# Performance work log

Hardware: AMD Instinct MI355X
Metric: run time of the kernel (lower is better)

The kernel has to match this reference:

```python
import jax, jax.numpy as jnp
import numpy as np

B, T, C = 2, 2048, 2048
N_HEAD = 16
N_KV_HEAD = 16
HEAD_DIM = C // N_HEAD  # 128
KV_LORA = C // 2        # 1024
KV_PE = KV_LORA // 4    # 256
KV_CONTENT = KV_LORA - KV_PE  # 768
EPS = 1.1920929e-07  # torch.finfo(float32).eps, F.rms_norm default


def _rms_norm(x):
    # unlearned RMSNorm over last dim
    return x * jax.lax.rsqrt(jnp.mean(x * x, axis=-1, keepdims=True) + EPS)


def _apply_rotary(x, cos, sin):
    # x: (B,T,H,D); cos,sin: (1,T,1,D/2)
    d = x.shape[-1] // 2
    x1, x2 = x[..., :d], x[..., d:]
    return jnp.concatenate([x1 * cos + x2 * sin, -x1 * sin + x2 * cos], axis=-1)


def setup_inputs() -> dict:
    key = jax.random.key(0)
    ks = jax.random.split(key, 9)
    x = jax.random.normal(ks[0], (B, T, C), dtype=jnp.float32)
    # realistic RoPE tables (values bounded like real cos/sin)
    half = HEAD_DIM // 2
    inv_freq = 1.0 / (10000.0 ** (np.arange(0, half, dtype=np.float32) / half))
    tpos = np.arange(T, dtype=np.float32)
    ang = np.einsum('t,d->td', tpos, inv_freq)
    cos = jnp.asarray(np.cos(ang))[None, :, None, :]
    sin = jnp.asarray(np.sin(ang))[None, :, None, :]
    s = 0.02
    wq_a = jax.random.normal(ks[1], (C, KV_LORA), dtype=jnp.float32) * s
    wq_b = jax.random.normal(ks[2], (KV_LORA, N_HEAD * HEAD_DIM), dtype=jnp.float32) * s
    wkv_a = jax.random.normal(ks[3], (C, KV_LORA), dtype=jnp.float32) * s
    wk_b = jax.random.normal(ks[4], (KV_CONTENT, N_KV_HEAD * HEAD_DIM), dtype=jnp.float32) * s
    wkpe_b = jax.random.normal(ks[5], (KV_PE, N_KV_HEAD * HEAD_DIM), dtype=jnp.float32) * s
    wv_b = jax.random.normal(ks[6], (KV_CONTENT, N_KV_HEAD * HEAD_DIM), dtype=jnp.float32) * s
    wo = jax.random.normal(ks[7], (C, C), dtype=jnp.float32) * s
    return dict(x=x, cos=cos, sin=sin, wq_a=wq_a, wq_b=wq_b, wkv_a=wkv_a,
                wk_b=wk_b, wkpe_b=wkpe_b, wv_b=wv_b, wo=wo)


def reference(x, cos, sin, wq_a, wq_b, wkv_a, wk_b, wkpe_b, wv_b, wo):
    Bx, Tx, Cx = x.shape
    # low-rank Q path
    q = (x @ wq_a) @ wq_b                      # (B,T,H*D)
    q = q.reshape(Bx, Tx, N_HEAD, HEAD_DIM)
    # low-rank KV path with pe/content split
    kv_latent = x @ wkv_a                       # (B,T,KV_LORA)
    kv_pe = kv_latent[..., :KV_PE]
    kv_content = kv_latent[..., KV_PE:]
    k_content = (kv_content @ wk_b).reshape(Bx, Tx, N_KV_HEAD, HEAD_DIM)
    k_pe = (kv_pe @ wkpe_b).reshape(Bx, Tx, N_KV_HEAD, HEAD_DIM)
    k = k_content + _apply_rotary(k_pe, cos, sin)
    v = (kv_content @ wv_b).reshape(Bx, Tx, N_KV_HEAD, HEAD_DIM)
    # QK RMSNorm (unlearned)
    q = _rms_norm(q)
    k = _rms_norm(k)
    # SDPA, causal (kv_cache=None path); n_head == n_kv_head
    qh = q.transpose(0, 2, 1, 3)  # (B,H,T,D)
    kh = k.transpose(0, 2, 1, 3)
    vh = v.transpose(0, 2, 1, 3)
    scale = 1.0 / jnp.sqrt(jnp.asarray(HEAD_DIM, dtype=x.dtype))
    scores = jnp.einsum('bhqd,bhkd->bhqk', qh, kh) * scale
    causal = jnp.tril(jnp.ones((Tx, Tx), dtype=bool))
    scores = jnp.where(causal[None, None], scores, jnp.asarray(-jnp.inf, dtype=scores.dtype))
    probs = jax.nn.softmax(scores, axis=-1)
    y = jnp.einsum('bhqk,bhkd->bhqd', probs, vh)
    y = y.transpose(0, 2, 1, 3).reshape(Bx, Tx, Cx)
    return y @ wo
```

## Files before the change

### kernel.cpp

```cpp
#include <hip/hip_runtime.h>
#include <cstddef>
#include <cstdint>

#define TT 2048
#define HH 16
#define EPSV 1.1920929e-07f
#define QSCALE 0.08838834764831845f
#define LOG2E 1.4426950408889634f
#define THRL 11.0f

typedef short bfv8 __attribute__((ext_vector_type(8)));
typedef short bfv4 __attribute__((ext_vector_type(4)));
typedef float f32x4 __attribute__((ext_vector_type(4)));
typedef unsigned u32x2 __attribute__((ext_vector_type(2)));

__device__ __forceinline__ short f2bf(float f) {
    unsigned u = __builtin_bit_cast(unsigned, f);
    u += 0x7FFFu + ((u >> 16) & 1u);
    return (short)(u >> 16);
}
__device__ __forceinline__ float bf2f(short s) {
    unsigned u = ((unsigned)(unsigned short)s) << 16;
    return __builtin_bit_cast(float, u);
}
__device__ __forceinline__ bfv8 pack8(const float4 a, const float4 b) {
    bfv8 r;
    r[0]=f2bf(a.x); r[1]=f2bf(a.y); r[2]=f2bf(a.z); r[3]=f2bf(a.w);
    r[4]=f2bf(b.x); r[5]=f2bf(b.y); r[6]=f2bf(b.z); r[7]=f2bf(b.w);
    return r;
}
__device__ __forceinline__ void gload16(const void* g, void* l) {
    __builtin_amdgcn_global_load_lds(
        (const __attribute__((address_space(1))) unsigned int*)g,
        (__attribute__((address_space(3))) unsigned int*)l, 16, 0, 0);
}
__device__ __forceinline__ unsigned cvtpk(float a, float b) {
    unsigned r;
    asm("v_cvt_pk_bf16_f32 %0, %1, %2" : "=v"(r) : "v"(a), "v"(b));
    return r;
}
__device__ __forceinline__ float fexp2(float x) {
    float y;
    asm volatile("v_exp_f32 %0, %1\n\ts_nop 1" : "=v"(y) : "v"(x));
    return y;
}
__device__ __forceinline__ float bperm(float v, int addr) {
    return __builtin_bit_cast(float,
        __builtin_amdgcn_ds_bpermute(addr, __builtin_bit_cast(int, v)));
}
__device__ __forceinline__ bfv4 mkfrag(float a, float b, float c, float d) {
    u32x2 t; t[0] = cvtpk(a, b); t[1] = cvtpk(c, d);
    return __builtin_bit_cast(bfv4, t);
}

struct TransDesc { const float* src; short* dst; int R, C, b0; };
struct TransArgs { TransDesc t[7]; };

__global__ __launch_bounds__(256) void pre_all(TransArgs ta,
    const float* __restrict__ xsrc, short* __restrict__ xdst, int nx)
{
    __shared__ short tile[64][72];
    int bid = blockIdx.x;
    if (bid < nx) {
        const int i = bid * 256 + threadIdx.x;
        float4 a = ((const float4*)xsrc)[2 * i], b = ((const float4*)xsrc)[2 * i + 1];
        ((bfv8*)xdst)[i] = pack8(a, b);
        return;
    }
    bid -= nx;
    int e = 0;
#pragma unroll
    for (int k = 1; k < 7; ++k) if (bid >= ta.t[k].b0) e = k;
    const TransDesc D = ta.t[e];
    const int loc = bid - D.b0;
    const int cb = D.C >> 6;
    const int by = loc / cb, bx = loc - by * cb;
    const int tid = threadIdx.x;
    const int r0 = by * 64, c0 = bx * 64;
    {
        const int i = tid >> 2, c = (tid & 3) * 16;
        const float* sp = D.src + ((size_t)(r0 + i)) * D.C + c0 + c;
        float4 v0 = ((const float4*)sp)[0], v1 = ((const float4*)sp)[1];
        float4 v2 = ((const float4*)sp)[2], v3 = ((const float4*)sp)[3];
        *(bfv8*)&tile[i][c]     = pack8(v0, v1);
        *(bfv8*)&tile[i][c + 8] = pack8(v2, v3);
    }
    __syncthreads();
    {
        const int j = tid >> 2, rc = (tid & 3) * 16;
        bfv8 g0, g1;
#pragma unroll
        for (int jj = 0; jj < 8; ++jj) { g0[jj] = tile[rc + jj][j]; g1[jj] = tile[rc + 8 + jj][j]; }
        short* dp = D.dst + ((size_t)(c0 + j)) * D.R + r0 + rc;
        *(bfv8*)dp       = g0;
        *(bfv8*)(dp + 8) = g1;
    }
}

template<int OUT_MODE>
__global__ __launch_bounds__(256) void gemm_bf16(
    const short* __restrict__ A, int lda,
    const short* __restrict__ B, int ldb,
    void* __restrict__ Cptr, int ldc, int K)
{
    __shared__ short As[2][128 * 32];
    __shared__ short Bs[2][128 * 32];
    const int tid = threadIdx.x;
    const int w = tid >> 6, lane = tid & 63;
    const int lr = lane & 15, lg = lane >> 4;
    const int wr = w >> 1, wc = w & 1;
    const size_t bm = (size_t)blockIdx.y * 128, bn = (size_t)blockIdx.x * 128;

    f32x4 acc[4][4] = {};

    const int r0 = tid >> 2, ch = (tid & 3) * 8;
    const short* aB0 = A + (bm + r0) * (size_t)lda + ch;
    const short* aB1 = aB0 + 64 * (size_t)lda;
    const short* bB0 = B + (bn + r0) * (size_t)ldb + ch;
    const short* bB1 = bB0 + 64 * (size_t)ldb;
    const int wof = w * 512;

    gload16(aB0, As[0] + wof);
    gload16(aB1, As[0] + wof + 2048);
    gload16(bB0, Bs[0] + wof);
    gload16(bB1, Bs[0] + wof + 2048);
    __syncthreads();

    int cur = 0;
    for (int k0 = 0; k0 < K; k0 += 32) {
        if (k0 + 32 < K) {
            gload16(aB0 + k0 + 32, As[cur ^ 1] + wof);
            gload16(aB1 + k0 + 32, As[cur ^ 1] + wof + 2048);
            gload16(bB0 + k0 + 32, Bs[cur ^ 1] + wof);
            gload16(bB1 + k0 + 32, Bs[cur ^ 1] + wof + 2048);
        }
        bfv8 af[4], bfr[4];
#pragma unroll
        for (int i = 0; i < 4; ++i) {
            af[i]  = *(const bfv8*)&As[cur][(wr * 64 + i * 16 + lr) * 32 + lg * 8];
            bfr[i] = *(const bfv8*)&Bs[cur][(wc * 64 + i * 16 + lr) * 32 + lg * 8];
        }
#pragma unroll
        for (int i = 0; i < 4; ++i)
#pragma unroll
            for (int j = 0; j < 4; ++j)
                acc[i][j] = __builtin_amdgcn_mfma_f32_16x16x32_bf16(af[i], bfr[j], acc[i][j], 0, 0, 0);
        __syncthreads();
        cur ^= 1;
    }

    if (OUT_MODE == 2) {
        short* out = (short*)Cptr;
        const size_t bb = bm >> 11;
        const int tb = (int)(bm & 2047) + wr * 64 + 4 * lg;
        const int colb = (int)bn + wc * 64 + lr;
#pragma unroll
        for (int i = 0; i < 4; ++i)
#pragma unroll
            for (int j = 0; j < 4; ++j) {
                const int c = colb + j * 16;
                const int h = c >> 7, d = c & 127;
                const size_t idx = (((bb * HH + h) * 128 + d) << 11) + tb + i * 16;
                *(bfv4*)&out[idx] = mkfrag(acc[i][j][0], acc[i][j][1], acc[i][j][2], acc[i][j][3]);
            }
    } else {
        const size_t crow = bm + wr * 64 + 4 * lg;
        const size_t ccol = bn + wc * 64 + lr;
#pragma unroll
        for (int i = 0; i < 4; ++i)
#pragma unroll
            for (int j = 0; j < 4; ++j)
#pragma unroll
                for (int r = 0; r < 4; ++r) {
                    size_t off = (crow + i * 16 + r) * (size_t)ldc + ccol + j * 16;
                    if (OUT_MODE == 0) ((float*)Cptr)[off] = acc[i][j][r];
                    else               ((short*)Cptr)[off] = f2bf(acc[i][j][r]);
                }
    }
}

__global__ __launch_bounds__(256) void finalize_k(
    const short* __restrict__ kc, const short* __restrict__ pe,
    const float* __restrict__ cosb, const float* __restrict__ sinb,
    short* __restrict__ kb)
{
    const int gw = blockIdx.x * 4 + (threadIdx.x >> 6);
    const int l = threadIdx.x & 63;
    const int r = gw >> 4, h = gw & 15;
    const int t = r & (TT - 1), b = r >> 11;
    const size_t kcb = (size_t)r * 2048 + h * 128;
    const size_t peb = (size_t)r * 2048 + h * 128;

    float x1 = bf2f(pe[peb + l]), x2 = bf2f(pe[peb + 64 + l]);
    float c = cosb[t * 64 + l], s = sinb[t * 64 + l];
    float lo = bf2f(kc[kcb + l])      + x1 * c + x2 * s;
    float hi = bf2f(kc[kcb + 64 + l]) - x1 * s + x2 * c;

    float ss = lo * lo + hi * hi;
#pragma unroll
    for (int o = 32; o; o >>= 1) ss += __shfl_xor(ss, o);
    float rr = rsqrtf(ss * (1.0f / 128.0f) + EPSV);
    const size_t ob = (((size_t)b * HH + h) * TT + t) * 128;
    kb[ob + l]      = f2bf(lo * rr);
    kb[ob + 64 + l] = f2bf(hi * rr);
}

__device__ __forceinline__ void qk_dual(const short* __restrict__ Ks,
    const bfv8 aq1[4], const bfv8 aq2[4], f32x4 s1[4], f32x4 s2[4], int lr, int lg)
{
    const int swz = lr & 7;
#pragma unroll
    for (int ct = 0; ct < 4; ++ct) {
        f32x4 a1 = {0.f, 0.f, 0.f, 0.f}, a2 = {0.f, 0.f, 0.f, 0.f};
        const int row = ct * 16 + lr;
#pragma unroll
        for (int ks = 0; ks < 4; ++ks) {
            const bfv8 bk = *(const bfv8*)&Ks[row * 128 + (((ks * 4 + lg) ^ swz) * 8)];
            a1 = __builtin_amdgcn_mfma_f32_16x16x32_bf16(bk, aq1[ks], a1, 0, 0, 0);
            a2 = __builtin_amdgcn_mfma_f32_16x16x32_bf16(bk, aq2[ks], a2, 0, 0, 0);
        }
        s1[ct] = a1; s2[ct] = a2;
    }
}

__device__ __forceinline__ void qk_one(const short* __restrict__ Ks,
    const bfv8 aq[4], f32x4 s[4], int lr, int lg)
{
    const int swz = lr & 7;
#pragma unroll
    for (int ct = 0; ct < 4; ++ct) {
        f32x4 a = {0.f, 0.f, 0.f, 0.f};
        const int row = ct * 16 + lr;
#pragma unroll
        for (int ks = 0; ks < 4; ++ks) {
            const bfv8 bk = *(const bfv8*)&Ks[row * 128 + (((ks * 4 + lg) ^ swz) * 8)];
            a = __builtin_amdgcn_mfma_f32_16x16x32_bf16(bk, aq[ks], a, 0, 0, 0);
        }
        s[ct] = a;
    }
}

__device__ __forceinline__ void mask_diag(f32x4 s[4], int lr, int lg, int w)
{
    const int qq = w * 16 + lr;
#pragma unroll
    for (int ct = 0; ct < 4; ++ct)
#pragma unroll
        for (int r = 0; r < 4; ++r)
            if (ct * 16 + 4 * lg + r > qq) s[ct][r] = -__builtin_inff();
}

__device__ __forceinline__ void softmax_lane(f32x4 s[4], float& m, float& l,
                                             f32x4 o[8], int a0)
{
    float c0 = fmaxf(fmaxf(s[0][0], s[0][1]), fmaxf(s[0][2], s[0][3]));
    float c1 = fmaxf(fmaxf(s[1][0], s[1][1]), fmaxf(s[1][2], s[1][3]));
    float c2 = fmaxf(fmaxf(s[2][0], s[2][1]), fmaxf(s[2][2], s[2][3]));
    float c3 = fmaxf(fmaxf(s[3][0], s[3][1]), fmaxf(s[3][2], s[3][3]));
    float mt = fmaxf(fmaxf(c0, c1), fmaxf(c2, c3));
    mt = fmaxf(mt, __shfl_xor(mt, 16));
    mt = fmaxf(mt, __shfl_xor(mt, 32));
    if (!__all(mt - m <= THRL)) {
        float mn = fmaxf(m, mt);
        float alpha = fexp2(m - mn);
        m = mn;
        l *= alpha;
        float av0 = bperm(alpha, a0);
        float av1 = bperm(alpha, a0 + 4);
        float av2 = bperm(alpha, a0 + 8);
        float av3 = bperm(alpha, a0 + 12);
#pragma unroll
        for (int dt = 0; dt < 8; ++dt) {
            o[dt][0] *= av0; o[dt][1] *= av1;
            o[dt][2] *= av2; o[dt][3] *= av3;
        }
    }
    f32x4 acc = {0.f, 0.f, 0.f, 0.f};
#pragma unroll
    for (int ct = 0; ct < 4; ++ct) {
#pragma unroll
        for (int r = 0; r < 4; ++r) s[ct][r] = fexp2(s[ct][r] - m);
        acc += s[ct];
    }
    float rs = (acc[0] + acc[1]) + (acc[2] + acc[3]);
    rs += __shfl_xor(rs, 16);
    rs += __shfl_xor(rs, 32);
    l += rs;
}

__device__ __forceinline__ void p_store(short (&Psw)[16][72], const f32x4 s[4],
                                        int lr, int lg)
{
#pragma unroll
    for (int ct = 0; ct < 4; ++ct)
        *(bfv4*)&Psw[lr][ct * 16 + 4 * lg] = mkfrag(s[ct][0], s[ct][1], s[ct][2], s[ct][3]);
}

__device__ __forceinline__ void pv_dual(const short* __restrict__ Vs,
    const short (&P1)[16][72], const short (&P2)[16][72],
    f32x4 o1[8], f32x4 o2[8], int lr, int lg)
{
    const bfv8 pa0 = *(const bfv8*)&P1[lr][lg * 8];
    const bfv8 pa1 = *(const bfv8*)&P1[lr][32 + lg * 8];
    const bfv8 pb0 = *(const bfv8*)&P2[lr][lg * 8];
    const bfv8 pb1 = *(const bfv8*)&P2[lr][32 + lg * 8];
    const int swz = lr & 7;
#pragma unroll
    for (int dt = 0; dt < 8; ++dt) {
        const int row = dt * 16 + lr;
        const bfv8 bv0 = *(const bfv8*)&Vs[row * 64 + ((lg ^ swz) * 8)];
        const bfv8 bv1 = *(const bfv8*)&Vs[row * 64 + (((4 + lg) ^ swz) * 8)];
        o1[dt] = __builtin_amdgcn_mfma_f32_16x16x32_bf16(pa0, bv0, o1[dt], 0, 0, 0);
        o1[dt] = __builtin_amdgcn_mfma_f32_16x16x32_bf16(pa1, bv1, o1[dt], 0, 0, 0);
        o2[dt] = __builtin_amdgcn_mfma_f32_16x16x32_bf16(pb0, bv0, o2[dt], 0, 0, 0);
        o2[dt] = __builtin_amdgcn_mfma_f32_16x16x32_bf16(pb1, bv1, o2[dt], 0, 0, 0);
    }
}

__device__ __forceinline__ void pv_one(const short* __restrict__ Vs,
    const short (&P2)[16][72], f32x4 o[8], int lr, int lg)
{
    const bfv8 pa0 = *(const bfv8*)&P2[lr][lg * 8];
    const bfv8 pa1 = *(const bfv8*)&P2[lr][32 + lg * 8];
    const int swz = lr & 7;
#pragma unroll
    for (int dt = 0; dt < 8; ++dt) {
        const int row = dt * 16 + lr;
        const bfv8 bv0 = *(const bfv8*)&Vs[row * 64 + ((lg ^ swz) * 8)];
        const bfv8 bv1 = *(const bfv8*)&Vs[row * 64 + (((4 + lg) ^ swz) * 8)];
        o[dt] = __builtin_amdgcn_mfma_f32_16x16x32_bf16(pa0, bv0, o[dt], 0, 0, 0);
        o[dt] = __builtin_amdgcn_mfma_f32_16x16x32_bf16(pa1, bv1, o[dt], 0, 0, 0);
    }
}

__global__ __launch_bounds__(256) void attn_kernel(
    const short* __restrict__ qg, const short* __restrict__ kg,
    const short* __restrict__ vg, short* __restrict__ y)
{
    __shared__ short Ks[64 * 128];
    __shared__ short Vs[128 * 64];
    __shared__ short Ps1[4][16][72];
    __shared__ short Ps2[4][16][72];

    const int lin = blockIdx.x + 16 * blockIdx.y + 256 * blockIdx.z;
    const int work = (lin & 7) * 64 + (lin >> 3);
    const int pi = work & 15, h = (work >> 4) & 15, b = work >> 8;
    const int qt1 = pi, qt2 = 31 - pi;
    const int tid = threadIdx.x, w = tid >> 6, lane = tid & 63;
    const int lr = lane & 15, lg = lane >> 4;
    const int a0 = lg * 80;

    const size_t tok0 = ((size_t)b * HH + h) * TT;

    bfv8 aq1[4], aq2[4];
    {
        const size_t q1 = ((size_t)b * TT + qt1 * 64 + w * 16 + lr) * 2048 + h * 128;
        const size_t q2 = ((size_t)b * TT + qt2 * 64 + w * 16 + lr) * 2048 + h * 128;
#pragma unroll
        for (int ks = 0; ks < 4; ++ks) {
            aq1[ks] = *(const bfv8*)&qg[q1 + ks * 32 + lg * 8];
            aq2[ks] = *(const bfv8*)&qg[q2 + ks * 32 + lg * 8];
        }
#pragma unroll
        for (int st = 0; st < 2; ++st) {
            bfv8* aq = st ? aq2 : aq1;
            float ss = 0.f;
#pragma unroll
            for (int ks = 0; ks < 4; ++ks)
#pragma unroll
                for (int j = 0; j < 8; ++j) { float f = bf2f(aq[ks][j]); ss = fmaf(f, f, ss); }
            ss += __shfl_xor(ss, 16);
            ss += __shfl_xor(ss, 32);
            float rr = rsqrtf(ss * (1.0f / 128.0f) + EPSV) * (QSCALE * LOG2E);
#pragma unroll
            for (int ks = 0; ks < 4; ++ks)
#pragma unroll
                for (int j = 0; j < 4; ++j) {
                    unsigned u = cvtpk(bf2f(aq[ks][2 * j]) * rr, bf2f(aq[ks][2 * j + 1]) * rr);
                    aq[ks][2 * j]     = (short)u;
                    aq[ks][2 * j + 1] = (short)(u >> 16);
                }
        }
    }

    f32x4 o1[8] = {}; f32x4 o2[8] = {};
    float m1 = -__builtin_inff(), m2 = -__builtin_inff();
    float l1 = 0.f, l2 = 0.f;

    const size_t vhead = ((size_t)b * HH + h) * (size_t)128 * TT;
    const int krow = tid >> 4, kub = (tid & 15) ^ (krow & 7);
    const int vrow = tid >> 3, vub = (tid & 7) ^ (vrow & 7);
    const int wof = w * 512;

    for (int kt = 0; kt <= qt2; ++kt) {
        {
            const size_t kbase = (tok0 + kt * 64) * 128;
#pragma unroll
            for (int p = 0; p < 4; ++p) {
                gload16(kg + kbase + (p * 16 + krow) * 128 + kub * 8, Ks + wof + p * 2048);
                gload16(vg + vhead + (size_t)(p * 32 + vrow) * TT + kt * 64 + vub * 8,
                        Vs + wof + p * 2048);
            }
        }
        __syncthreads();

        if (kt <= qt1) {
            f32x4 s1[4], s2[4];
            qk_dual(Ks, aq1, aq2, s1, s2, lr, lg);
            if (kt == qt1) mask_diag(s1, lr, lg, w);
            softmax_lane(s1, m1, l1, o1, a0);
            softmax_lane(s2, m2, l2, o2, a0);
            p_store(Ps1[w], s1, lr, lg);
            p_store(Ps2[w], s2, lr, lg);
            pv_dual(Vs, Ps1[w], Ps2[w], o1, o2, lr, lg);
        } else {
            f32x4 s2[4];
            qk_one(Ks, aq2, s2, lr, lg);
            if (kt == qt2) mask_diag(s2, lr, lg, w);
            softmax_lane(s2, m2, l2, o2, a0);
            p_store(Ps2[w], s2, lr, lg);
            pv_one(Vs, Ps2[w], o2, lr, lg);
        }
        __syncthreads();
    }

    float n1 = 1.0f / l1, n2 = 1.0f / l2;
    float iv1[4], iv2[4];
#pragma unroll
    for (int r = 0; r < 4; ++r) {
        iv1[r] = bperm(n1, a0 + 4 * r);
        iv2[r] = bperm(n2, a0 + 4 * r);
    }
#pragma unroll
    for (int r = 0; r < 4; ++r) {
        const size_t y1 = ((size_t)b * TT + qt1 * 64 + w * 16 + 4 * lg + r) * 2048 + h * 128 + lr;
        const size_t y2 = ((size_t)b * TT + qt2 * 64 + w * 16 + 4 * lg + r) * 2048 + h * 128 + lr;
#pragma unroll
        for (int dt = 0; dt < 8; ++dt) {
            y[y1 + dt * 16] = f2bf(o1[dt][r] * iv1[r]);
            y[y2 + dt * 16] = f2bf(o2[dt][r] * iv2[r]);
        }
    }
}

extern "C" void kernel_launch(void* const* d_in, const int* in_sizes, int n_in,
                              void* d_out, int out_size, void* d_ws, size_t ws_size,
                              hipStream_t stream)
{
    const float* x      = (const float*)d_in[0];
    const float* cosb   = (const float*)d_in[1];
    const float* sinb   = (const float*)d_in[2];
    const float* wq_a   = (const float*)d_in[3];
    const float* wq_b   = (const float*)d_in[4];
    const float* wkv_a  = (const float*)d_in[5];
    const float* wk_b   = (const float*)d_in[6];
    const float* wkpe_b = (const float*)d_in[7];
    const float* wv_b   = (const float*)d_in[8];
    const float* wo     = (const float*)d_in[9];

    short* wsp = (short*)d_ws;
    short* W1  = wsp;
    short* W2  = wsp + 4194304;
    short* W3  = wsp + 7340032;
    short* W4  = wsp + 7864320;
    short* W5  = wsp + 9961472;
    short* C1  = wsp + 14155776;
    short* KC  = wsp + 22544384;
    short* KPE = wsp + 30932992;
    short* KB  = wsp + 39321600;
    short* VB  = wsp + 47710208;
    short* XB  = (short*)d_out;

    dim3 blk(256);

    TransArgs ta;
    ta.t[0] = {wq_a,   W1,                2048, 1024,    0};
    ta.t[1] = {wkv_a,  W1 + 1024 * 2048,  2048, 1024,  512};
    ta.t[2] = {wk_b,   W2,                 768, 2048, 1024};
    ta.t[3] = {wv_b,   W2 + 2048 * 768,    768, 2048, 1408};
    ta.t[4] = {wkpe_b, W3,                 256, 2048, 1792};
    ta.t[5] = {wq_b,   W4,                1024, 2048, 1920};
    ta.t[6] = {wo,     W5,                2048, 2048, 2432};
    pre_all<<<4096 + 3456, blk, 0, stream>>>(ta, x, XB, 4096);

    gemm_bf16<1><<<dim3(16, 32), blk, 0, stream>>>(XB, 2048, W1, 2048, C1, 2048, 2048);
    gemm_bf16<1><<<dim3(16, 32), blk, 0, stream>>>(C1 + 1280, 2048, W2, 768, KC, 2048, 768);
    gemm_bf16<2><<<dim3(16, 32), blk, 0, stream>>>(C1 + 1280, 2048, W2 + 2048 * 768, 768, VB, 0, 768);
    gemm_bf16<1><<<dim3(16, 32), blk, 0, stream>>>(C1 + 1024, 2048, W3, 256, KPE, 2048, 256);

    finalize_k<<<16384, blk, 0, stream>>>(KC, KPE, cosb, sinb, KB);

    gemm_bf16<1><<<dim3(16, 32), blk, 0, stream>>>(C1, 2048, W4, 1024, KPE, 2048, 1024);

    attn_kernel<<<dim3(16, 16, 2), blk, 0, stream>>>(KPE, KB, VB, C1);

    gemm_bf16<0><<<dim3(16, 32), blk, 0, stream>>>(C1, 2048, W5, 2048, d_out, 2048, 2048);
}
```

Baseline: 316.2 us.

## Fuse RoPE and K RMSNorm into the k_content GEMM epilogue

Replaces the separate k_content GEMM and finalize_k kernel with one GEMM whose epilogue adds the rotary k_pe term, computes the per-head RMS across the two column warps through shared memory, and writes normalized K directly in head-major layout. This drops the KC intermediate round trip through memory and one launch, at the cost of a heavier, scattered-read epilogue. It also changes the attention work mapping to pair adjacent query tiles in descending order instead of the balanced front/back pairing, which alters load balance across blocks.

```diff
diff --git a/kernel.cpp b/kernel.cpp
--- a/kernel.cpp
+++ b/kernel.cpp
@@ -179,30 +179,121 @@
     }
 }
 
-__global__ __launch_bounds__(256) void finalize_k(
-    const short* __restrict__ kc, const short* __restrict__ pe,
-    const float* __restrict__ cosb, const float* __restrict__ sinb,
-    short* __restrict__ kb)
-{
-    const int gw = blockIdx.x * 4 + (threadIdx.x >> 6);
-    const int l = threadIdx.x & 63;
-    const int r = gw >> 4, h = gw & 15;
-    const int t = r & (TT - 1), b = r >> 11;
-    const size_t kcb = (size_t)r * 2048 + h * 128;
-    const size_t peb = (size_t)r * 2048 + h * 128;
-
-    float x1 = bf2f(pe[peb + l]), x2 = bf2f(pe[peb + 64 + l]);
-    float c = cosb[t * 64 + l], s = sinb[t * 64 + l];
-    float lo = bf2f(kc[kcb + l])      + x1 * c + x2 * s;
-    float hi = bf2f(kc[kcb + 64 + l]) - x1 * s + x2 * c;
-
-    float ss = lo * lo + hi * hi;
-#pragma unroll
-    for (int o = 32; o; o >>= 1) ss += __shfl_xor(ss, o);
-    float rr = rsqrtf(ss * (1.0f / 128.0f) + EPSV);
-    const size_t ob = (((size_t)b * HH + h) * TT + t) * 128;
-    kb[ob + l]      = f2bf(lo * rr);
-    kb[ob + 64 + l] = f2bf(hi * rr);
+__global__ __launch_bounds__(256) void gemm_kc_rope(
+    const short* __restrict__ A, int lda,
+    const short* __restrict__ B, int ldb,
+    const short* __restrict__ KPE,
+    const float* __restrict__ cosb,
+    const float* __restrict__ sinb,
+    short* __restrict__ KB, int K)
+{
+    __shared__ short As[2][128 * 32];
+    __shared__ short Bs[2][128 * 32];
+    const int tid = threadIdx.x;
+    const int w = tid >> 6, lane = tid & 63;
+    const int lr = lane & 15, lg = lane >> 4;
+    const int wr = w >> 1, wc = w & 1;
+    const size_t bm = (size_t)blockIdx.y * 128, bn = (size_t)blockIdx.x * 128;
+
+    f32x4 acc[4][4] = {};
+
+    const int r0 = tid >> 2, ch = (tid & 3) * 8;
+    const short* aB0 = A + (bm + r0) * (size_t)lda + ch;
+    const short* aB1 = aB0 + 64 * (size_t)lda;
+    const short* bB0 = B + (bn + r0) * (size_t)ldb + ch;
+    const short* bB1 = bB0 + 64 * (size_t)ldb;
+    const int wof = w * 512;
+
+    gload16(aB0, As[0] + wof);
+    gload16(aB1, As[0] + wof + 2048);
+    gload16(bB0, Bs[0] + wof);
+    gload16(bB1, Bs[0] + wof + 2048);
+    __syncthreads();
+
+    int cur = 0;
+    for (int k0 = 0; k0 < K; k0 += 32) {
+        if (k0 + 32 < K) {
+            gload16(aB0 + k0 + 32, As[cur ^ 1] + wof);
+            gload16(aB1 + k0 + 32, As[cur ^ 1] + wof + 2048);
+            gload16(bB0 + k0 + 32, Bs[cur ^ 1] + wof);
+            gload16(bB1 + k0 + 32, Bs[cur ^ 1] + wof + 2048);
+        }
+        bfv8 af[4], bfr[4];
+#pragma unroll
+        for (int i = 0; i < 4; ++i) {
+            af[i]  = *(const bfv8*)&As[cur][(wr * 64 + i * 16 + lr) * 32 + lg * 8];
+            bfr[i] = *(const bfv8*)&Bs[cur][(wc * 64 + i * 16 + lr) * 32 + lg * 8];
+        }
+#pragma unroll
+        for (int i = 0; i < 4; ++i)
+#pragma unroll
+            for (int j = 0; j < 4; ++j)
+                acc[i][j] = __builtin_amdgcn_mfma_f32_16x16x32_bf16(af[i], bfr[j], acc[i][j], 0, 0, 0);
+        __syncthreads();
+        cur ^= 1;
+    }
+
+    const int hh = (int)(bn >> 7);
+#pragma unroll
+    for (int i = 0; i < 4; ++i)
+#pragma unroll
+        for (int r = 0; r < 4; ++r) {
+            const int R = (int)bm + wr * 64 + i * 16 + 4 * lg + r;
+            const int t = R & (TT - 1);
+#pragma unroll
+            for (int j = 0; j < 4; ++j) {
+                const int colg = (int)bn + wc * 64 + j * 16 + lr;
+                const int d64  = j * 16 + lr;
+                const float pe_self = bf2f(KPE[(size_t)R * 2048 + colg]);
+                const float pe_part = bf2f(KPE[(size_t)R * 2048 + colg + (wc ? -64 : 64)]);
+                const float c = cosb[t * 64 + d64], s = sinb[t * 64 + d64];
+                const float rope = wc ? (pe_self * c - pe_part * s)
+                                      : (pe_self * c + pe_part * s);
+                acc[i][j][r] += rope;
+            }
+        }
+
+    float ps[4][4];
+#pragma unroll
+    for (int i = 0; i < 4; ++i)
+#pragma unroll
+        for (int r = 0; r < 4; ++r) {
+            float v = acc[i][0][r] * acc[i][0][r];
+            v = fmaf(acc[i][1][r], acc[i][1][r], v);
+            v = fmaf(acc[i][2][r], acc[i][2][r], v);
+            v = fmaf(acc[i][3][r], acc[i][3][r], v);
+            ps[i][r] = v;
+        }
+#pragma unroll
+    for (int off = 1; off < 16; off <<= 1)
+#pragma unroll
+        for (int i = 0; i < 4; ++i)
+#pragma unroll
+            for (int r = 0; r < 4; ++r) ps[i][r] += __shfl_xor(ps[i][r], off);
+
+    float* rbuf = (float*)As;
+    if (lr == 0) {
+#pragma unroll
+        for (int i = 0; i < 4; ++i)
+#pragma unroll
+            for (int r = 0; r < 4; ++r)
+                rbuf[((wc * 2 + wr) * 4 + lg) * 16 + i * 4 + r] = ps[i][r];
+    }
+    __syncthreads();
+
+#pragma unroll
+    for (int i = 0; i < 4; ++i)
+#pragma unroll
+        for (int r = 0; r < 4; ++r) {
+            const float tot = ps[i][r] + rbuf[(((wc ^ 1) * 2 + wr) * 4 + lg) * 16 + i * 4 + r];
+            const float rr = rsqrtf(tot * (1.0f / 128.0f) + EPSV);
+            const int R = (int)bm + wr * 64 + i * 16 + 4 * lg + r;
+            const int t = R & (TT - 1), bb = R >> 11;
+            const size_t ob = (((size_t)bb * HH + hh) * TT + t) * 128 + wc * 64 + lr;
+#pragma unroll
+            for (int j = 0; j < 4; ++j)
+                KB[ob + j * 16] = f2bf(acc[i][j][r] * rr);
+        }
 }
 
 __device__ __forceinline__ void qk_dual(const short* __restrict__ Ks,
@@ -344,8 +435,9 @@
 
     const int lin = blockIdx.x + 16 * blockIdx.y + 256 * blockIdx.z;
     const int work = (lin & 7) * 64 + (lin >> 3);
-    const int pi = work & 15, h = (work >> 4) & 15, b = work >> 8;
-    const int qt1 = pi, qt2 = 31 - pi;
+    const int pi = 15 - (work & 15);
+    const int h = (work >> 4) & 15, b = work >> 8;
+    const int qt1 = 2 * pi, qt2 = 2 * pi + 1;
     const int tid = threadIdx.x, w = tid >> 6, lane = tid & 63;
     const int lr = lane & 15, lg = lane >> 4;
     const int a0 = lg * 80;
@@ -465,7 +557,6 @@
     short* W4  = wsp + 7864320;
     short* W5  = wsp + 9961472;
     short* C1  = wsp + 14155776;
-    short* KC  = wsp + 22544384;
     short* KPE = wsp + 30932992;
     short* KB  = wsp + 39321600;
     short* VB  = wsp + 47710208;
@@ -484,11 +575,10 @@
     pre_all<<<4096 + 3456, blk, 0, stream>>>(ta, x, XB, 4096);
 
     gemm_bf16<1><<<dim3(16, 32), blk, 0, stream>>>(XB, 2048, W1, 2048, C1, 2048, 2048);
-    gemm_bf16<1><<<dim3(16, 32), blk, 0, stream>>>(C1 + 1280, 2048, W2, 768, KC, 2048, 768);
+    gemm_bf16<1><<<dim3(16, 32), blk, 0, stream>>>(C1 + 1024, 2048, W3, 256, KPE, 2048, 256);
+    gemm_kc_rope<<<dim3(16, 32), blk, 0, stream>>>(C1 + 1280, 2048, W2, 768,
+                                                   KPE, cosb, sinb, KB, 768);
     gemm_bf16<2><<<dim3(16, 32), blk, 0, stream>>>(C1 + 1280, 2048, W2 + 2048 * 768, 768, VB, 0, 768);
-    gemm_bf16<1><<<dim3(16, 32), blk, 0, stream>>>(C1 + 1024, 2048, W3, 256, KPE, 2048, 256);
-
-    finalize_k<<<16384, blk, 0, stream>>>(KC, KPE, cosb, sinb, KB);
 
     gemm_bf16<1><<<dim3(16, 32), blk, 0, stream>>>(C1, 2048, W4, 1024, KPE, 2048, 1024);
 
```

Measured after the change: 349.9 us. 1.11x slower.

## Split causal attention KV range across two blocks and merge partial outputs

Applied to the files above, without the earlier changes.

Each (batch, head, q-tile pair) work item is split into two blocks, each covering roughly half of the key range. Each block writes unnormalized bf16 partial outputs plus its running max and sum, and a new merge kernel rescales and combines them. This doubles the number of attention blocks to improve occupancy and latency hiding across the CUs. The cost is an extra kernel launch, extra partial-output traffic, and rounding the unnormalized accumulators to bf16.

```diff
diff --git a/kernel.cpp b/kernel.cpp
--- a/kernel.cpp
+++ b/kernel.cpp
@@ -43,10 +43,6 @@
     float y;
     asm volatile("v_exp_f32 %0, %1\n\ts_nop 1" : "=v"(y) : "v"(x));
     return y;
-}
-__device__ __forceinline__ float bperm(float v, int addr) {
-    return __builtin_bit_cast(float,
-        __builtin_amdgcn_ds_bpermute(addr, __builtin_bit_cast(int, v)));
 }
 __device__ __forceinline__ bfv4 mkfrag(float a, float b, float c, float d) {
     u32x2 t; t[0] = cvtpk(a, b); t[1] = cvtpk(c, d);
@@ -265,10 +261,10 @@
         float alpha = fexp2(m - mn);
         m = mn;
         l *= alpha;
-        float av0 = bperm(alpha, a0);
-        float av1 = bperm(alpha, a0 + 4);
-        float av2 = bperm(alpha, a0 + 8);
-        float av3 = bperm(alpha, a0 + 12);
+        float av0 = __builtin_bit_cast(float, __builtin_amdgcn_ds_bpermute(a0,      __builtin_bit_cast(int, alpha)));
+        float av1 = __builtin_bit_cast(float, __builtin_amdgcn_ds_bpermute(a0 + 4,  __builtin_bit_cast(int, alpha)));
+        float av2 = __builtin_bit_cast(float, __builtin_amdgcn_ds_bpermute(a0 + 8,  __builtin_bit_cast(int, alpha)));
+        float av3 = __builtin_bit_cast(float, __builtin_amdgcn_ds_bpermute(a0 + 12, __builtin_bit_cast(int, alpha)));
 #pragma unroll
         for (int dt = 0; dt < 8; ++dt) {
             o[dt][0] *= av0; o[dt][1] *= av1;
@@ -333,19 +329,24 @@
     }
 }
 
-__global__ __launch_bounds__(256) void attn_kernel(
+__global__ __launch_bounds__(256) void attn_split(
     const short* __restrict__ qg, const short* __restrict__ kg,
-    const short* __restrict__ vg, short* __restrict__ y)
+    const short* __restrict__ vg,
+    short* __restrict__ po0, short* __restrict__ po1,
+    float* __restrict__ ml)
 {
     __shared__ short Ks[64 * 128];
     __shared__ short Vs[128 * 64];
     __shared__ short Ps1[4][16][72];
     __shared__ short Ps2[4][16][72];
 
-    const int lin = blockIdx.x + 16 * blockIdx.y + 256 * blockIdx.z;
-    const int work = (lin & 7) * 64 + (lin >> 3);
-    const int pi = work & 15, h = (work >> 4) & 15, b = work >> 8;
+    const int lin = blockIdx.x + 32 * blockIdx.y + 512 * blockIdx.z;
+    const int work = (lin & 7) * 128 + (lin >> 3);
+    const int s = work & 1;
+    const int pi = (work >> 1) & 15;
+    const int h = (work >> 5) & 15, b = work >> 9;
     const int qt1 = pi, qt2 = 31 - pi;
+    const int h1 = (qt1 + 2) >> 1, h2 = (qt2 + 2) >> 1;
     const int tid = threadIdx.x, w = tid >> 6, lane = tid & 63;
     const int lr = lane & 15, lg = lane >> 4;
     const int a0 = lg * 80;
@@ -392,55 +393,111 @@
     const int vrow = tid >> 3, vub = (tid & 7) ^ (vrow & 7);
     const int wof = w * 512;
 
-    for (int kt = 0; kt <= qt2; ++kt) {
-        {
-            const size_t kbase = (tok0 + kt * 64) * 128;
-#pragma unroll
-            for (int p = 0; p < 4; ++p) {
-                gload16(kg + kbase + (p * 16 + krow) * 128 + kub * 8, Ks + wof + p * 2048);
-                gload16(vg + vhead + (size_t)(p * 32 + vrow) * TT + kt * 64 + vub * 8,
-                        Vs + wof + p * 2048);
-            }
-        }
-        __syncthreads();
-
-        if (kt <= qt1) {
-            f32x4 s1[4], s2[4];
-            qk_dual(Ks, aq1, aq2, s1, s2, lr, lg);
-            if (kt == qt1) mask_diag(s1, lr, lg, w);
-            softmax_lane(s1, m1, l1, o1, a0);
-            softmax_lane(s2, m2, l2, o2, a0);
-            p_store(Ps1[w], s1, lr, lg);
-            p_store(Ps2[w], s2, lr, lg);
-            pv_dual(Vs, Ps1[w], Ps2[w], o1, o2, lr, lg);
-        } else {
-            f32x4 s2[4];
-            qk_one(Ks, aq2, s2, lr, lg);
-            if (kt == qt2) mask_diag(s2, lr, lg, w);
-            softmax_lane(s2, m2, l2, o2, a0);
-            p_store(Ps2[w], s2, lr, lg);
-            pv_one(Vs, Ps2[w], o2, lr, lg);
-        }
-        __syncthreads();
-    }
-
-    float n1 = 1.0f / l1, n2 = 1.0f / l2;
-    float iv1[4], iv2[4];
+#define STAGE_T(KT)                                                                 \
+    {                                                                               \
+        const size_t kbase = (tok0 + (KT) * 64) * 128;                              \
+        _Pragma("unroll")                                                           \
+        for (int p = 0; p < 4; ++p) {                                               \
+            gload16(kg + kbase + (p * 16 + krow) * 128 + kub * 8, Ks + wof + p * 2048); \
+            gload16(vg + vhead + (size_t)(p * 32 + vrow) * TT + (KT) * 64 + vub * 8,    \
+                    Vs + wof + p * 2048);                                           \
+        }                                                                           \
+    }
+
+#define STEP_DUAL(KT)                                                  \
+    {                                                                  \
+        f32x4 s1[4], s2[4];                                            \
+        qk_dual(Ks, aq1, aq2, s1, s2, lr, lg);                         \
+        if ((KT) == qt1) mask_diag(s1, lr, lg, w);                     \
+        softmax_lane(s1, m1, l1, o1, a0);                              \
+        softmax_lane(s2, m2, l2, o2, a0);                              \
+        p_store(Ps1[w], s1, lr, lg);                                   \
+        p_store(Ps2[w], s2, lr, lg);                                   \
+        pv_dual(Vs, Ps1[w], Ps2[w], o1, o2, lr, lg);                   \
+    }
+#define STEP_S1(KT)                                                    \
+    {                                                                  \
+        f32x4 s1[4];                                                   \
+        qk_one(Ks, aq1, s1, lr, lg);                                   \
+        if ((KT) == qt1) mask_diag(s1, lr, lg, w);                     \
+        softmax_lane(s1, m1, l1, o1, a0);                              \
+        p_store(Ps1[w], s1, lr, lg);                                   \
+        pv_one(Vs, Ps1[w], o1, lr, lg);                                \
+    }
+#define STEP_S2(KT)                                                    \
+    {                                                                  \
+        f32x4 s2[4];                                                   \
+        qk_one(Ks, aq2, s2, lr, lg);                                   \
+        if ((KT) == qt2) mask_diag(s2, lr, lg, w);                     \
+        softmax_lane(s2, m2, l2, o2, a0);                              \
+        p_store(Ps2[w], s2, lr, lg);                                   \
+        pv_one(Vs, Ps2[w], o2, lr, lg);                                \
+    }
+
+    if (s == 0) {
+        for (int kt = 0; kt < h1; ++kt) {
+            STAGE_T(kt); __syncthreads();
+            STEP_DUAL(kt); __syncthreads();
+        }
+        for (int kt = h1; kt < h2; ++kt) {
+            STAGE_T(kt); __syncthreads();
+            STEP_S2(kt); __syncthreads();
+        }
+    } else {
+        const int e1 = (qt1 < h2 - 1) ? qt1 : (h2 - 1);
+        for (int kt = h1; kt <= e1; ++kt) {
+            STAGE_T(kt); __syncthreads();
+            STEP_S1(kt); __syncthreads();
+        }
+        for (int kt = h2; kt <= qt2; ++kt) {
+            STAGE_T(kt); __syncthreads();
+            if (kt <= qt1) STEP_DUAL(kt) else STEP_S2(kt);
+            __syncthreads();
+        }
+    }
+
+    short* po = s ? po1 : po0;
+    const int row1 = ((b * HH + h) * TT) + qt1 * 64 + w * 16;
+    const int row2 = ((b * HH + h) * TT) + qt2 * 64 + w * 16;
+    if (lg == 0) {
+        ml[(size_t)(s * 65536 + row1 + lr) * 2]     = m1;
+        ml[(size_t)(s * 65536 + row1 + lr) * 2 + 1] = l1;
+        ml[(size_t)(s * 65536 + row2 + lr) * 2]     = m2;
+        ml[(size_t)(s * 65536 + row2 + lr) * 2 + 1] = l2;
+    }
 #pragma unroll
     for (int r = 0; r < 4; ++r) {
-        iv1[r] = bperm(n1, a0 + 4 * r);
-        iv2[r] = bperm(n2, a0 + 4 * r);
-    }
-#pragma unroll
-    for (int r = 0; r < 4; ++r) {
-        const size_t y1 = ((size_t)b * TT + qt1 * 64 + w * 16 + 4 * lg + r) * 2048 + h * 128 + lr;
-        const size_t y2 = ((size_t)b * TT + qt2 * 64 + w * 16 + 4 * lg + r) * 2048 + h * 128 + lr;
+        const size_t p1 = (size_t)(row1 + 4 * lg + r) * 128 + lr;
+        const size_t p2 = (size_t)(row2 + 4 * lg + r) * 128 + lr;
 #pragma unroll
         for (int dt = 0; dt < 8; ++dt) {
-            y[y1 + dt * 16] = f2bf(o1[dt][r] * iv1[r]);
-            y[y2 + dt * 16] = f2bf(o2[dt][r] * iv2[r]);
-        }
-    }
+            po[p1 + dt * 16] = f2bf(o1[dt][r]);
+            po[p2 + dt * 16] = f2bf(o2[dt][r]);
+        }
+    }
+}
+
+__global__ __launch_bounds__(256) void attn_merge(
+    const short* __restrict__ po0, const short* __restrict__ po1,
+    const float* __restrict__ ml, short* __restrict__ y)
+{
+    const int idx8 = blockIdx.x * 256 + threadIdx.x;
+    const int row = idx8 >> 4;
+    const int d0 = (idx8 & 15) * 8;
+    const float m0 = ml[(size_t)row * 2], l0 = ml[(size_t)row * 2 + 1];
+    const float m1 = ml[(size_t)(65536 + row) * 2], l1 = ml[(size_t)(65536 + row) * 2 + 1];
+    const float mm = fmaxf(m0, m1);
+    const float a0 = exp2f(m0 - mm), a1 = exp2f(m1 - mm);
+    const float inv = 1.0f / (l0 * a0 + l1 * a1);
+    const float f0 = a0 * inv, f1 = a1 * inv;
+    const bfv8 p0 = *(const bfv8*)&po0[(size_t)row * 128 + d0];
+    const bfv8 p1 = *(const bfv8*)&po1[(size_t)row * 128 + d0];
+    bfv8 r;
+#pragma unroll
+    for (int j = 0; j < 8; ++j)
+        r[j] = f2bf(bf2f(p0[j]) * f0 + bf2f(p1[j]) * f1);
+    const int bb = row >> 15, hh = (row >> 11) & 15, t = row & 2047;
+    *(bfv8*)&y[(((size_t)bb * TT + t) * 2048) + hh * 128 + d0] = r;
 }
 
 extern "C" void kernel_launch(void* const* d_in, const int* in_sizes, int n_in,
@@ -469,6 +526,9 @@
     short* KPE = wsp + 30932992;
     short* KB  = wsp + 39321600;
     short* VB  = wsp + 47710208;
+    short* PO0 = wsp;
+    short* PO1 = KC;
+    float* ML  = (float*)(wsp + 56098816);
     short* XB  = (short*)d_out;
 
     dim3 blk(256);
@@ -492,7 +552,8 @@
 
     gemm_bf16<1><<<dim3(16, 32), blk, 0, stream>>>(C1, 2048, W4, 1024, KPE, 2048, 1024);
 
-    attn_kernel<<<dim3(16, 16, 2), blk, 0, stream>>>(KPE, KB, VB, C1);
+    attn_split<<<dim3(32, 16, 2), blk, 0, stream>>>(KPE, KB, VB, PO0, PO1, ML);
+    attn_merge<<<4096, blk, 0, stream>>>(PO0, PO1, ML, C1);
 
     gemm_bf16<0><<<dim3(16, 32), blk, 0, stream>>>(C1, 2048, W5, 2048, d_out, 2048, 2048);
 }
```

Measured after the change: 315.9 us. About the same (-0.1%).
